# Performance work log

Measured on AMD Instinct MI355X. Metric: run time of the kernel, lower is better.

The kernel has to match this reference:

```python
import jax, jax.numpy as jnp
import numpy as np
from jax import lax

EPS = 1e-5
TEM = 10.0  # self.tem at init; tem_proportion buffer is 0 so it stays 10.0


def _conv1d(x, w, padding, dilation=1, groups=1):
    # x: [B, C, S], w: [O, I//groups, K]
    return lax.conv_general_dilated(
        x, w, window_strides=(1,), padding=[(padding, padding)],
        rhs_dilation=(dilation,), dimension_numbers=('NCH', 'OIH', 'NCH'),
        feature_group_count=groups)


def _bn(y, gamma, beta):
    # training-mode BatchNorm1d: stats over (batch, length) per channel
    m = y.mean(axis=(0, 2), keepdims=True)
    v = y.var(axis=(0, 2), keepdims=True)
    return (y - m) * lax.rsqrt(v + EPS) * gamma[None, :, None] + beta[None, :, None]


def _nor_conv(x, w, g, b, k):
    return _bn(_conv1d(jax.nn.relu(x), w, padding=k // 2), g, b)


def _dil_conv(x, wd, wp, g, b, k):
    C = x.shape[1]
    y = _conv1d(jax.nn.relu(x), wd, padding=k - 1, dilation=2, groups=C)
    y = _conv1d(y, wp, padding=0)
    return _bn(y, g, b)


def _avg_pool3(x):
    s = lax.reduce_window(x, 0.0, lax.add, (1, 1, 3), (1, 1, 1),
                          [(0, 0), (0, 0), (1, 1)])
    return s / 3.0  # count_include_pad=True


def _max_pool3(x):
    return lax.reduce_window(x, -jnp.inf, lax.max, (1, 1, 3), (1, 1, 1),
                             [(0, 0), (0, 0), (1, 1)])


def _forward(x, u, arch_parameters,
             w_nor3, g_nor3, b_nor3, w_nor5, g_nor5, b_nor5,
             w_nor7, g_nor7, b_nor7,
             wd_dil3, wp_dil3, g_dil3, b_dil3,
             wd_dil5, wp_dil5, g_dil5, b_dil5,
             wd_dil7, wp_dil7, g_dil7, b_dil7):
    # ---- Gumbel straight-through gate (get_gumbel_prob) ----
    uc = jnp.clip(u, 1e-9, 1.0 - 1e-9)
    gumbels = -jnp.log(-jnp.log(uc))  # -log(Exp(1) sample)
    logits = (jax.nn.log_softmax(arch_parameters, axis=1) + gumbels) / TEM
    probs = jax.nn.softmax(logits, axis=1)          # [1, 10]
    index = jnp.argmax(probs, axis=-1)              # [1]
    one_h = jax.nn.one_hot(index, probs.shape[-1], dtype=probs.dtype)
    hardwts = one_h - lax.stop_gradient(probs) + probs  # straight-through

    # ---- forward_gdas: single edge (max_nodes=2) ----
    xc = jnp.transpose(x, (0, 2, 1))  # [B, H, S]: hidden=channels, seq=length
    branches = [
        lambda t: jnp.zeros_like(t),                         # none
        _avg_pool3,                                          # avg_pool_3
        _max_pool3,                                          # max_pool_3
        lambda t: _nor_conv(t, w_nor3, g_nor3, b_nor3, 3),   # nor_conv_3
        lambda t: _nor_conv(t, w_nor5, g_nor5, b_nor5, 5),   # nor_conv_5
        lambda t: _nor_conv(t, w_nor7, g_nor7, b_nor7, 7),   # nor_conv_7
        lambda t: _dil_conv(t, wd_dil3, wp_dil3, g_dil3, b_dil3, 3),
        lambda t: _dil_conv(t, wd_dil5, wp_dil5, g_dil5, b_dil5, 5),
        lambda t: _dil_conv(t, wd_dil7, wp_dil7, g_dil7, b_dil7, 7),
        lambda t: t,                                         # skip_connect
    ]
    idx = index[0]
    w = hardwts[0]                                  # [10]
    sel = lax.switch(idx, branches, xc)             # only argmax op is run
    w_sel = jnp.take(w, idx)
    # GDAS: w[argmax]*op(x) + sum of remaining scalar weights (broadcast add)
    out = w_sel * sel + (jnp.sum(w) - w_sel)
    out = jnp.transpose(out, (0, 2, 1))             # back to [B, S, H]
    return out + x                                  # residual


def setup_inputs() -> dict:
    key = jax.random.key(0)
    ks = jax.random.split(key, 16)
    B, S, H = 8, 512, 768
    d = {
        'x': jax.random.normal(ks[0], (B, S, H), jnp.float32),
        'u': jax.random.uniform(ks[1], (1, 10), jnp.float32),
        'arch_parameters': 0.001 * jax.random.normal(ks[2], (1, 10), jnp.float32),
    }
    i = 3
    for k in (3, 5, 7):
        d[f'w_nor{k}'] = 0.02 * jax.random.normal(ks[i], (H, H, k), jnp.float32); i += 1
        d[f'g_nor{k}'] = jnp.ones((H,), jnp.float32)
        d[f'b_nor{k}'] = jnp.zeros((H,), jnp.float32)
    for k in (3, 5, 7):
        d[f'wd_dil{k}'] = 0.1 * jax.random.normal(ks[i], (H, 1, k), jnp.float32); i += 1
        d[f'wp_dil{k}'] = 0.02 * jax.random.normal(ks[i], (H, H, 1), jnp.float32); i += 1
        d[f'g_dil{k}'] = jnp.ones((H,), jnp.float32)
        d[f'b_dil{k}'] = jnp.zeros((H,), jnp.float32)
    return d


def reference(x, u, arch_parameters,
              w_nor3, g_nor3, b_nor3, w_nor5, g_nor5, b_nor5,
              w_nor7, g_nor7, b_nor7,
              wd_dil3, wp_dil3, g_dil3, b_dil3,
              wd_dil5, wp_dil5, g_dil5, b_dil5,
              wd_dil7, wp_dil7, g_dil7, b_dil7):
    return _forward(x, u, arch_parameters,
                    w_nor3, g_nor3, b_nor3, w_nor5, g_nor5, b_nor5,
                    w_nor7, g_nor7, b_nor7,
                    wd_dil3, wp_dil3, g_dil3, b_dil3,
                    wd_dil5, wp_dil5, g_dil5, b_dil5,
                    wd_dil7, wp_dil7, g_dil7, b_dil7)
```

## Files before the change

kernel.cpp:

```cpp
#include <hip/hip_runtime.h>
#include <math.h>

#define BB 8
#define SS 512
#define HH 768
#define NTOT (BB*SS*HH)
#define EPSBN 1e-5f

struct Params {
  const float *x, *u, *ap;
  const float *w_nor3, *g_nor3, *b_nor3;
  const float *w_nor5, *g_nor5, *b_nor5;
  const float *w_nor7, *g_nor7, *b_nor7;
  const float *wd3, *wp3, *gd3, *bd3;
  const float *wd5, *wp5, *gd5, *bd5;
  const float *wd7, *wp7, *gd7, *bd7;
  float *out;
  float *hdr;
  float *y;
  float *z;
  float *psum;
  float *psq;
  float *mbuf;
  float *ibuf;
};

__global__ void gate_kernel(Params p) {
  if (threadIdx.x != 0 || blockIdx.x != 0) return;
  float ap[10], lg[10], pr[10];
  float mx = -INFINITY;
  for (int i = 0; i < 10; i++) { ap[i] = p.ap[i]; mx = fmaxf(mx, ap[i]); }
  float se = 0.f;
  for (int i = 0; i < 10; i++) se += expf(ap[i] - mx);
  float lse = mx + logf(se);
  float lmax = -INFINITY;
  for (int i = 0; i < 10; i++) {
    float uc = fminf(fmaxf(p.u[i], 1e-9f), 1.f - 1e-9f);
    float gb = -logf(-logf(uc));
    lg[i] = ((ap[i] - lse) + gb) * 0.1f;
    lmax = fmaxf(lmax, lg[i]);
  }
  float ps = 0.f;
  for (int i = 0; i < 10; i++) { pr[i] = expf(lg[i] - lmax); ps += pr[i]; }
  int idx = 0; float best = -INFINITY;
  for (int i = 0; i < 10; i++) {
    pr[i] /= ps;
    if (pr[i] > best) { best = pr[i]; idx = i; }
  }
  float w_sel = (1.0f - pr[idx]) + pr[idx];
  p.hdr[0] = w_sel;
  p.hdr[1] = 0.0f;
  ((int*)p.hdr)[2] = idx;
}

__global__ __launch_bounds__(256) void simple_kernel(Params p) {
  int idx = ((const int*)p.hdr)[2];
  if (idx >= 3 && idx <= 8) return;
  float w_sel = p.hdr[0], w_rest = p.hdr[1];
  int tid = blockIdx.x * 256 + threadIdx.x;
  if (tid >= NTOT) return;
  int bs = tid / HH;
  int s = bs % SS;
  float xv = p.x[tid];
  float sel;
  if (idx == 0) sel = 0.f;
  else if (idx == 9) sel = xv;
  else if (idx == 1) {
    float xm = (s > 0) ? p.x[tid - HH] : 0.f;
    float xp = (s < SS - 1) ? p.x[tid + HH] : 0.f;
    sel = (xm + xv + xp) * (1.f / 3.f);
  } else {
    float xm = (s > 0) ? p.x[tid - HH] : -INFINITY;
    float xp = (s < SS - 1) ? p.x[tid + HH] : -INFINITY;
    sel = fmaxf(fmaxf(xm, xv), xp);
  }
  p.out[tid] = w_sel * sel + w_rest + xv;
}

__global__ __launch_bounds__(256) void dw_kernel(Params p) {
  int idx = ((const int*)p.hdr)[2];
  if (idx < 6 || idx > 8) return;
  int k = 3 + 2 * (idx - 6);
  const float* wd = (idx == 6) ? p.wd3 : (idx == 7) ? p.wd5 : p.wd7;
  int tid = blockIdx.x * 256 + threadIdx.x;
  if (tid >= NTOT) return;
  int c = tid % HH;
  int bs = tid / HH;
  int s = bs % SS;
  int b = bs / SS;
  float acc = 0.f;
  for (int dk = 0; dk < k; dk++) {
    int ss = s + 2 * dk - (k - 1);
    if (ss >= 0 && ss < SS) {
      float v = p.x[((size_t)(b * SS + ss)) * HH + c];
      acc += fmaxf(v, 0.f) * wd[c * k + dk];
    }
  }
  p.z[tid] = acc;
}

#define TM 64
#define TN 64
#define TK 16
__global__ __launch_bounds__(256) void conv_gemm_kernel(Params p) {
  int idx = ((const int*)p.hdr)[2];
  if (idx < 3 || idx > 8) return;
  bool nor = (idx <= 5);
  int k = nor ? (3 + 2 * (idx - 3)) : (3 + 2 * (idx - 6));
  const float* W = nor ? ((idx == 3) ? p.w_nor3 : (idx == 4) ? p.w_nor5 : p.w_nor7)
                       : ((idx == 6) ? p.wp3 : (idx == 7) ? p.wp5 : p.wp7);
  const float* A = nor ? p.x : p.z;
  int taps = nor ? k : 1;
  int halo = nor ? (k >> 1) : 0;

  __shared__ float As[TK][TM + 4];
  __shared__ float Bs[TK][TN + 4];

  int bm = blockIdx.x;
  int b = bm >> 3;
  int s0 = (bm & 7) * TM;
  int o0 = blockIdx.y * TN;

  int t = threadIdx.x;
  int lkk = t & 15;
  int lr = t >> 4;
  int tm0 = (t & 15) * 4;
  int tn0 = (t >> 4) * 4;

  float acc[4][4];
#pragma unroll
  for (int i = 0; i < 4; i++)
#pragma unroll
    for (int j = 0; j < 4; j++) acc[i][j] = 0.f;

  for (int dk = 0; dk < taps; dk++) {
    int shift = dk - halo;
    for (int i0 = 0; i0 < HH; i0 += TK) {
#pragma unroll
      for (int r = 0; r < 4; r++) {
        int m = lr + 16 * r;
        int srow = s0 + m + shift;
        float v = 0.f;
        if (srow >= 0 && srow < SS) {
          float raw = A[((size_t)(b * SS + srow)) * HH + i0 + lkk];
          v = nor ? fmaxf(raw, 0.f) : raw;
        }
        As[lkk][m] = v;
      }
#pragma unroll
      for (int r = 0; r < 4; r++) {
        int o = o0 + lr + 16 * r;
        float wv = nor ? W[((size_t)o * HH + i0 + lkk) * k + dk]
                       : W[(size_t)o * HH + i0 + lkk];
        Bs[lkk][lr + 16 * r] = wv;
      }
      __syncthreads();
#pragma unroll
      for (int kk = 0; kk < TK; kk++) {
        float4 a = *(const float4*)&As[kk][tm0];
        float4 bv = *(const float4*)&Bs[kk][tn0];
        acc[0][0] += a.x * bv.x; acc[0][1] += a.x * bv.y; acc[0][2] += a.x * bv.z; acc[0][3] += a.x * bv.w;
        acc[1][0] += a.y * bv.x; acc[1][1] += a.y * bv.y; acc[1][2] += a.y * bv.z; acc[1][3] += a.y * bv.w;
        acc[2][0] += a.z * bv.x; acc[2][1] += a.z * bv.y; acc[2][2] += a.z * bv.z; acc[2][3] += a.z * bv.w;
        acc[3][0] += a.w * bv.x; acc[3][1] += a.w * bv.y; acc[3][2] += a.w * bv.z; acc[3][3] += a.w * bv.w;
      }
      __syncthreads();
    }
  }
#pragma unroll
  for (int mi = 0; mi < 4; mi++) {
    int m = tm0 + mi;
#pragma unroll
    for (int ni = 0; ni < 4; ni++) {
      p.y[((size_t)(b * SS + s0 + m)) * HH + o0 + tn0 + ni] = acc[mi][ni];
    }
  }
}

__global__ __launch_bounds__(256) void bn_stats1(Params p) {
  int idx = ((const int*)p.hdr)[2];
  if (idx < 3 || idx > 8) return;
  int t = threadIdx.x;
  int c = blockIdx.y * 64 + (t & 63);
  int rsub = t >> 6;
  float s = 0.f, q = 0.f;
  int rbase = blockIdx.x * 256 + rsub;
  for (int j = 0; j < 64; j++) {
    float v = p.y[(size_t)(rbase + 4 * j) * HH + c];
    s += v; q += v * v;
  }
  __shared__ float red[2][4][64];
  red[0][rsub][t & 63] = s;
  red[1][rsub][t & 63] = q;
  __syncthreads();
  if (t < 64) {
    float ts = red[0][0][t] + red[0][1][t] + red[0][2][t] + red[0][3][t];
    float tq = red[1][0][t] + red[1][1][t] + red[1][2][t] + red[1][3][t];
    p.psum[blockIdx.x * HH + blockIdx.y * 64 + t] = ts;
    p.psq[blockIdx.x * HH + blockIdx.y * 64 + t] = tq;
  }
}

__global__ __launch_bounds__(256) void bn_stats2(Params p) {
  int idx = ((const int*)p.hdr)[2];
  if (idx < 3 || idx > 8) return;
  int c = blockIdx.x * 256 + threadIdx.x;
  if (c >= HH) return;
  float s = 0.f, q = 0.f;
  for (int j = 0; j < 16; j++) { s += p.psum[j * HH + c]; q += p.psq[j * HH + c]; }
  float mean = s * (1.f / 4096.f);
  float var = q * (1.f / 4096.f) - mean * mean;
  p.mbuf[c] = mean;
  p.ibuf[c] = rsqrtf(var + EPSBN);
}

__global__ __launch_bounds__(256) void finalize_kernel(Params p) {
  int idx = ((const int*)p.hdr)[2];
  if (idx < 3 || idx > 8) return;
  const float* g = (idx == 3) ? p.g_nor3 : (idx == 4) ? p.g_nor5 : (idx == 5) ? p.g_nor7
                 : (idx == 6) ? p.gd3 : (idx == 7) ? p.gd5 : p.gd7;
  const float* be = (idx == 3) ? p.b_nor3 : (idx == 4) ? p.b_nor5 : (idx == 5) ? p.b_nor7
                  : (idx == 6) ? p.bd3 : (idx == 7) ? p.bd5 : p.bd7;
  float w_sel = p.hdr[0], w_rest = p.hdr[1];
  int tid = blockIdx.x * 256 + threadIdx.x;
  if (tid >= NTOT) return;
  int h = tid % HH;
  float yv = p.y[tid];
  float nv = (yv - p.mbuf[h]) * p.ibuf[h] * g[h] + be[h];
  p.out[tid] = w_sel * nv + w_rest + p.x[tid];
}

extern "C" void kernel_launch(void* const* d_in, const int* in_sizes, int n_in,
                              void* d_out, int out_size, void* d_ws, size_t ws_size,
                              hipStream_t stream) {
  Params p;
  p.x = (const float*)d_in[0];
  p.u = (const float*)d_in[1];
  p.ap = (const float*)d_in[2];
  p.w_nor3 = (const float*)d_in[3];  p.g_nor3 = (const float*)d_in[4];  p.b_nor3 = (const float*)d_in[5];
  p.w_nor5 = (const float*)d_in[6];  p.g_nor5 = (const float*)d_in[7];  p.b_nor5 = (const float*)d_in[8];
  p.w_nor7 = (const float*)d_in[9];  p.g_nor7 = (const float*)d_in[10]; p.b_nor7 = (const float*)d_in[11];
  p.wd3 = (const float*)d_in[12]; p.wp3 = (const float*)d_in[13]; p.gd3 = (const float*)d_in[14]; p.bd3 = (const float*)d_in[15];
  p.wd5 = (const float*)d_in[16]; p.wp5 = (const float*)d_in[17]; p.gd5 = (const float*)d_in[18]; p.bd5 = (const float*)d_in[19];
  p.wd7 = (const float*)d_in[20]; p.wp7 = (const float*)d_in[21]; p.gd7 = (const float*)d_in[22]; p.bd7 = (const float*)d_in[23];
  p.out = (float*)d_out;

  char* ws = (char*)d_ws;
  size_t off = 0;
  p.hdr = (float*)(ws + off); off += 256;
  p.y   = (float*)(ws + off); off += (size_t)NTOT * 4;
  p.z   = (float*)(ws + off); off += (size_t)NTOT * 4;
  p.psum = (float*)(ws + off); off += 16 * HH * 4;
  p.psq  = (float*)(ws + off); off += 16 * HH * 4;
  p.mbuf = (float*)(ws + off); off += HH * 4;
  p.ibuf = (float*)(ws + off); off += HH * 4;

  int nblk = (NTOT + 255) / 256;

  hipLaunchKernelGGL(gate_kernel, dim3(1), dim3(64), 0, stream, p);
  hipLaunchKernelGGL(simple_kernel, dim3(nblk), dim3(256), 0, stream, p);
  hipLaunchKernelGGL(dw_kernel, dim3(nblk), dim3(256), 0, stream, p);
  hipLaunchKernelGGL(conv_gemm_kernel, dim3(BB * SS / TM, HH / TN), dim3(256), 0, stream, p);
  hipLaunchKernelGGL(bn_stats1, dim3(16, HH / 64), dim3(256), 0, stream, p);
  hipLaunchKernelGGL(bn_stats2, dim3((HH + 255) / 256), dim3(256), 0, stream, p);
  hipLaunchKernelGGL(finalize_kernel, dim3(nblk), dim3(256), 0, stream, p);
}
```

Baseline: 147.6 us.

## Use bf16 MFMA tiles for conv GEMM and merge simple path into epilogue

Replaces the fp32 scalar-FMA tiled GEMM with a 128x64x32 tiled kernel that converts activations and weights to bf16 in shared memory and computes with 16x16x32 bf16 MFMA instructions. It also folds the separate simple-op kernel into the final epilogue kernel, removing one full-grid launch. Using bf16 inputs lowers precision of the convolution, and the nor-path weight loads stay strided and uncoalesced.

```diff
diff --git a/kernel.cpp b/kernel.cpp
--- a/kernel.cpp
+++ b/kernel.cpp
@@ -6,6 +6,9 @@
 #define HH 768
 #define NTOT (BB*SS*HH)
 #define EPSBN 1e-5f
+
+typedef __attribute__((ext_vector_type(8))) short short8v;
+typedef __attribute__((ext_vector_type(4))) float float4v;
 
 struct Params {
   const float *x, *u, *ap;
@@ -25,6 +28,12 @@
   float *ibuf;
 };
 
+__device__ __forceinline__ short f2bf(float f) {
+  union { float f; unsigned u; } v; v.f = f;
+  unsigned r = v.u + 0x7FFF + ((v.u >> 16) & 1);
+  return (short)(r >> 16);
+}
+
 __global__ void gate_kernel(Params p) {
   if (threadIdx.x != 0 || blockIdx.x != 0) return;
   float ap[10], lg[10], pr[10];
@@ -51,30 +60,6 @@
   p.hdr[0] = w_sel;
   p.hdr[1] = 0.0f;
   ((int*)p.hdr)[2] = idx;
-}
-
-__global__ __launch_bounds__(256) void simple_kernel(Params p) {
-  int idx = ((const int*)p.hdr)[2];
-  if (idx >= 3 && idx <= 8) return;
-  float w_sel = p.hdr[0], w_rest = p.hdr[1];
-  int tid = blockIdx.x * 256 + threadIdx.x;
-  if (tid >= NTOT) return;
-  int bs = tid / HH;
-  int s = bs % SS;
-  float xv = p.x[tid];
-  float sel;
-  if (idx == 0) sel = 0.f;
-  else if (idx == 9) sel = xv;
-  else if (idx == 1) {
-    float xm = (s > 0) ? p.x[tid - HH] : 0.f;
-    float xp = (s < SS - 1) ? p.x[tid + HH] : 0.f;
-    sel = (xm + xv + xp) * (1.f / 3.f);
-  } else {
-    float xm = (s > 0) ? p.x[tid - HH] : -INFINITY;
-    float xp = (s < SS - 1) ? p.x[tid + HH] : -INFINITY;
-    sel = fmaxf(fmaxf(xm, xv), xp);
-  }
-  p.out[tid] = w_sel * sel + w_rest + xv;
 }
 
 __global__ __launch_bounds__(256) void dw_kernel(Params p) {
@@ -99,9 +84,10 @@
   p.z[tid] = acc;
 }
 
-#define TM 64
-#define TN 64
-#define TK 16
+#define BM 128
+#define BN 64
+#define BK 32
+#define LROW 40
 __global__ __launch_bounds__(256) void conv_gemm_kernel(Params p) {
   int idx = ((const int*)p.hdr)[2];
   if (idx < 3 || idx > 8) return;
@@ -113,66 +99,105 @@
   int taps = nor ? k : 1;
   int halo = nor ? (k >> 1) : 0;
 
-  __shared__ float As[TK][TM + 4];
-  __shared__ float Bs[TK][TN + 4];
-
-  int bm = blockIdx.x;
-  int b = bm >> 3;
-  int s0 = (bm & 7) * TM;
-  int o0 = blockIdx.y * TN;
+  __shared__ __attribute__((aligned(16))) short As[BM * LROW];
+  __shared__ __attribute__((aligned(16))) short Bs[BN * LROW];
+
+  int mt = blockIdx.x;
+  int b = mt >> 2;
+  int s0 = (mt & 3) * BM;
+  int o0 = blockIdx.y * BN;
 
   int t = threadIdx.x;
-  int lkk = t & 15;
-  int lr = t >> 4;
-  int tm0 = (t & 15) * 4;
-  int tn0 = (t >> 4) * 4;
-
-  float acc[4][4];
-#pragma unroll
-  for (int i = 0; i < 4; i++)
-#pragma unroll
-    for (int j = 0; j < 4; j++) acc[i][j] = 0.f;
+  int lane = t & 63;
+  int wid = t >> 6;
+  int wm0 = (wid >> 1) * 64;
+  int wn0 = (wid & 1) * 32;
+  int l16 = lane & 15;
+  int quad = lane >> 4;
+
+  int sa_m = t >> 1;
+  int sa_h = t & 1;
+  int sb_n = t >> 2;
+  int sb_seg = t & 3;
+
+  float4v acc[4][2];
+#pragma unroll
+  for (int mi = 0; mi < 4; mi++)
+#pragma unroll
+    for (int ni = 0; ni < 2; ni++) acc[mi][ni] = (float4v){0.f, 0.f, 0.f, 0.f};
 
   for (int dk = 0; dk < taps; dk++) {
     int shift = dk - halo;
-    for (int i0 = 0; i0 < HH; i0 += TK) {
-#pragma unroll
-      for (int r = 0; r < 4; r++) {
-        int m = lr + 16 * r;
-        int srow = s0 + m + shift;
-        float v = 0.f;
+    for (int k0 = 0; k0 < HH; k0 += BK) {
+      {
+        int srow = s0 + sa_m + shift;
+        float4 f[4];
         if (srow >= 0 && srow < SS) {
-          float raw = A[((size_t)(b * SS + srow)) * HH + i0 + lkk];
-          v = nor ? fmaxf(raw, 0.f) : raw;
+          const float* ap = A + ((size_t)(b * SS + srow)) * HH + k0 + sa_h * 16;
+#pragma unroll
+          for (int j = 0; j < 4; j++) f[j] = ((const float4*)ap)[j];
+        } else {
+#pragma unroll
+          for (int j = 0; j < 4; j++) f[j] = (float4){0.f, 0.f, 0.f, 0.f};
         }
-        As[lkk][m] = v;
+        short h16[16];
+#pragma unroll
+        for (int j = 0; j < 4; j++) {
+          float vx = f[j].x, vy = f[j].y, vz = f[j].z, vw = f[j].w;
+          if (nor) { vx = fmaxf(vx, 0.f); vy = fmaxf(vy, 0.f); vz = fmaxf(vz, 0.f); vw = fmaxf(vw, 0.f); }
+          h16[4 * j + 0] = f2bf(vx); h16[4 * j + 1] = f2bf(vy);
+          h16[4 * j + 2] = f2bf(vz); h16[4 * j + 3] = f2bf(vw);
+        }
+        short* dst = &As[sa_m * LROW + sa_h * 16];
+        *(short8v*)dst = *(short8v*)&h16[0];
+        *(short8v*)(dst + 8) = *(short8v*)&h16[8];
       }
-#pragma unroll
-      for (int r = 0; r < 4; r++) {
-        int o = o0 + lr + 16 * r;
-        float wv = nor ? W[((size_t)o * HH + i0 + lkk) * k + dk]
-                       : W[(size_t)o * HH + i0 + lkk];
-        Bs[lkk][lr + 16 * r] = wv;
+      {
+        short h8[8];
+        int o = o0 + sb_n;
+        if (!nor) {
+          const float* bp = W + (size_t)o * HH + k0 + sb_seg * 8;
+          float4 f0 = ((const float4*)bp)[0];
+          float4 f1 = ((const float4*)bp)[1];
+          h8[0] = f2bf(f0.x); h8[1] = f2bf(f0.y); h8[2] = f2bf(f0.z); h8[3] = f2bf(f0.w);
+          h8[4] = f2bf(f1.x); h8[5] = f2bf(f1.y); h8[6] = f2bf(f1.z); h8[7] = f2bf(f1.w);
+        } else {
+#pragma unroll
+          for (int j = 0; j < 8; j++) {
+            int i = k0 + sb_seg * 8 + j;
+            h8[j] = f2bf(W[((size_t)o * HH + i) * k + dk]);
+          }
+        }
+        *(short8v*)&Bs[sb_n * LROW + sb_seg * 8] = *(short8v*)&h8[0];
       }
       __syncthreads();
-#pragma unroll
-      for (int kk = 0; kk < TK; kk++) {
-        float4 a = *(const float4*)&As[kk][tm0];
-        float4 bv = *(const float4*)&Bs[kk][tn0];
-        acc[0][0] += a.x * bv.x; acc[0][1] += a.x * bv.y; acc[0][2] += a.x * bv.z; acc[0][3] += a.x * bv.w;
-        acc[1][0] += a.y * bv.x; acc[1][1] += a.y * bv.y; acc[1][2] += a.y * bv.z; acc[1][3] += a.y * bv.w;
-        acc[2][0] += a.z * bv.x; acc[2][1] += a.z * bv.y; acc[2][2] += a.z * bv.z; acc[2][3] += a.z * bv.w;
-        acc[3][0] += a.w * bv.x; acc[3][1] += a.w * bv.y; acc[3][2] += a.w * bv.z; acc[3][3] += a.w * bv.w;
-      }
+
+      short8v af[4], bf[2];
+#pragma unroll
+      for (int mi = 0; mi < 4; mi++)
+        af[mi] = *(const short8v*)&As[(wm0 + mi * 16 + l16) * LROW + quad * 8];
+#pragma unroll
+      for (int ni = 0; ni < 2; ni++)
+        bf[ni] = *(const short8v*)&Bs[(wn0 + ni * 16 + l16) * LROW + quad * 8];
+#pragma unroll
+      for (int mi = 0; mi < 4; mi++)
+#pragma unroll
+        for (int ni = 0; ni < 2; ni++)
+          acc[mi][ni] = __builtin_amdgcn_mfma_f32_16x16x32_bf16(af[mi], bf[ni], acc[mi][ni], 0, 0, 0);
       __syncthreads();
     }
   }
+
 #pragma unroll
   for (int mi = 0; mi < 4; mi++) {
-    int m = tm0 + mi;
-#pragma unroll
-    for (int ni = 0; ni < 4; ni++) {
-      p.y[((size_t)(b * SS + s0 + m)) * HH + o0 + tn0 + ni] = acc[mi][ni];
+#pragma unroll
+    for (int ni = 0; ni < 2; ni++) {
+      int col = o0 + wn0 + ni * 16 + l16;
+#pragma unroll
+      for (int r = 0; r < 4; r++) {
+        int row = s0 + wm0 + mi * 16 + quad * 4 + r;
+        p.y[((size_t)(b * SS + row)) * HH + col] = acc[mi][ni][r];
+      }
     }
   }
 }
@@ -214,20 +239,39 @@
   p.ibuf[c] = rsqrtf(var + EPSBN);
 }
 
-__global__ __launch_bounds__(256) void finalize_kernel(Params p) {
-  int idx = ((const int*)p.hdr)[2];
-  if (idx < 3 || idx > 8) return;
-  const float* g = (idx == 3) ? p.g_nor3 : (idx == 4) ? p.g_nor5 : (idx == 5) ? p.g_nor7
-                 : (idx == 6) ? p.gd3 : (idx == 7) ? p.gd5 : p.gd7;
-  const float* be = (idx == 3) ? p.b_nor3 : (idx == 4) ? p.b_nor5 : (idx == 5) ? p.b_nor7
-                  : (idx == 6) ? p.bd3 : (idx == 7) ? p.bd5 : p.bd7;
+__global__ __launch_bounds__(256) void epilogue_kernel(Params p) {
+  int idx = ((const int*)p.hdr)[2];
   float w_sel = p.hdr[0], w_rest = p.hdr[1];
   int tid = blockIdx.x * 256 + threadIdx.x;
   if (tid >= NTOT) return;
-  int h = tid % HH;
-  float yv = p.y[tid];
-  float nv = (yv - p.mbuf[h]) * p.ibuf[h] * g[h] + be[h];
-  p.out[tid] = w_sel * nv + w_rest + p.x[tid];
+  float xv = p.x[tid];
+  float sel;
+  if (idx >= 3 && idx <= 8) {
+    const float* g = (idx == 3) ? p.g_nor3 : (idx == 4) ? p.g_nor5 : (idx == 5) ? p.g_nor7
+                   : (idx == 6) ? p.gd3 : (idx == 7) ? p.gd5 : p.gd7;
+    const float* be = (idx == 3) ? p.b_nor3 : (idx == 4) ? p.b_nor5 : (idx == 5) ? p.b_nor7
+                    : (idx == 6) ? p.bd3 : (idx == 7) ? p.bd5 : p.bd7;
+    int h = tid % HH;
+    float yv = p.y[tid];
+    sel = (yv - p.mbuf[h]) * p.ibuf[h] * g[h] + be[h];
+  } else if (idx == 0) {
+    sel = 0.f;
+  } else if (idx == 9) {
+    sel = xv;
+  } else {
+    int bs = tid / HH;
+    int s = bs % SS;
+    if (idx == 1) {
+      float xm = (s > 0) ? p.x[tid - HH] : 0.f;
+      float xp = (s < SS - 1) ? p.x[tid + HH] : 0.f;
+      sel = (xm + xv + xp) * (1.f / 3.f);
+    } else {
+      float xm = (s > 0) ? p.x[tid - HH] : -INFINITY;
+      float xp = (s < SS - 1) ? p.x[tid + HH] : -INFINITY;
+      sel = fmaxf(fmaxf(xm, xv), xp);
+    }
+  }
+  p.out[tid] = w_sel * sel + w_rest + xv;
 }
 
 extern "C" void kernel_launch(void* const* d_in, const int* in_sizes, int n_in,
@@ -258,10 +302,9 @@
   int nblk = (NTOT + 255) / 256;
 
   hipLaunchKernelGGL(gate_kernel, dim3(1), dim3(64), 0, stream, p);
-  hipLaunchKernelGGL(simple_kernel, dim3(nblk), dim3(256), 0, stream, p);
   hipLaunchKernelGGL(dw_kernel, dim3(nblk), dim3(256), 0, stream, p);
-  hipLaunchKernelGGL(conv_gemm_kernel, dim3(BB * SS / TM, HH / TN), dim3(256), 0, stream, p);
+  hipLaunchKernelGGL(conv_gemm_kernel, dim3(32, HH / BN), dim3(256), 0, stream, p);
   hipLaunchKernelGGL(bn_stats1, dim3(16, HH / 64), dim3(256), 0, stream, p);
   hipLaunchKernelGGL(bn_stats2, dim3((HH + 255) / 256), dim3(256), 0, stream, p);
-  hipLaunchKernelGGL(finalize_kernel, dim3(nblk), dim3(256), 0, stream, p);
-}
+  hipLaunchKernelGGL(epilogue_kernel, dim3(nblk), dim3(256), 0, stream, p);
+}
```

New measurement: 144.7 us. 1.02x faster.
